# Kernel optimization log

Hardware: AMD Instinct MI355X
Metric: run time of the kernel (lower is better)

The kernel has to match this reference:

```python
import jax, jax.numpy as jnp
import numpy as np

B, T, C, H, W = 1, 16, 320, 16, 16
HEADS, DIM_HEAD, NREG = 8, 40, 1
L = T * H * W  # 4096


def setup_inputs() -> dict:
    key = jax.random.key(0)
    ks = jax.random.split(key, 8)
    features = jax.random.normal(ks[0], (B, T, C, H, W), jnp.float32)
    # epipolar geometry mask: True = attend. randint 0/1 per spec.
    attn_mask = jax.random.randint(ks[1], (B, L, L), 0, 2) == 1
    s = 0.02
    Wq = jax.random.normal(ks[2], (C, HEADS * DIM_HEAD), jnp.float32) * s
    Wk = jax.random.normal(ks[3], (C, HEADS * DIM_HEAD), jnp.float32) * s
    Wv = jax.random.normal(ks[4], (C, HEADS * DIM_HEAD), jnp.float32) * s
    reg_tokens = jax.random.normal(ks[5], (1, NREG, C), jnp.float32)
    Wo = jax.random.normal(ks[6], (HEADS * DIM_HEAD, C), jnp.float32) * s
    bo = jnp.zeros((C,), jnp.float32)
    return {"features": features, "attn_mask": attn_mask, "Wq": Wq, "Wk": Wk,
            "Wv": Wv, "reg_tokens": reg_tokens, "Wo": Wo, "bo": bo}


def reference(features, attn_mask, Wq, Wk, Wv, reg_tokens, Wo, bo):
    b, t, c, h, w = features.shape
    # B T C H W -> B (T H W) C
    x = features.transpose(0, 1, 3, 4, 2).reshape(b, t * h * w, c)
    context = jnp.concatenate(
        [jnp.broadcast_to(reg_tokens, (b, NREG, c)), x], axis=1)
    # pad mask: register tokens always visible (True)
    mask = jnp.pad(attn_mask, ((0, 0), (0, 0), (NREG, 0)), constant_values=True)
    # projections, split heads: B L (H D) -> B H L D
    def heads(y):
        return y.reshape(b, y.shape[1], HEADS, DIM_HEAD).transpose(0, 2, 1, 3)
    q = heads(x @ Wq)
    k = heads(context @ Wk)
    v = heads(context @ Wv)
    scale = DIM_HEAD ** -0.5  # SDPA default scale
    scores = jnp.einsum('bhqd,bhkd->bhqk', q, k) * scale
    neg = jnp.finfo(scores.dtype).min
    scores = jnp.where(mask[:, None, :, :], scores, neg)
    attn = jax.nn.softmax(scores, axis=-1)
    out = jnp.einsum('bhqk,bhkd->bhqd', attn, v)
    out = out.transpose(0, 2, 1, 3).reshape(b, t * h * w, HEADS * DIM_HEAD)
    out = out @ Wo + bo
    # B (T H W) C -> (B H W) T C
    out = out.reshape(b, t, h, w, c).transpose(0, 2, 3, 1, 4)
    return out.reshape(b * h * w, t, c)
```

## Files before the change

kernel.cpp:

```cpp
#include <hip/hip_runtime.h>
#include <hip/hip_bf16.h>
#include <math.h>

#define CDIM 320
#define LQ   4096
#define LKTX 4097
#define NH   8
#define DH   40
#define NWORDS 65
#define NSPLIT 2

typedef __attribute__((ext_vector_type(8))) short short8;
typedef __attribute__((ext_vector_type(4))) float f32x4;

#define QSCALE ((float)(0.15811388300841897 * 1.4426950408889634))


__global__ __launch_bounds__(256) void prep(
    const float* __restrict__ feat, const float* __restrict__ reg,
    const float* __restrict__ Wq, const float* __restrict__ Wk,
    const float* __restrict__ Wv, const float* __restrict__ Wo,
    __hip_bfloat16* __restrict__ ctxb, __hip_bfloat16* __restrict__ Wt,
    __hip_bfloat16* __restrict__ Wot, short* __restrict__ Kpack,
    short* __restrict__ Vpack) {
    __shared__ float xs[64 * 65];
    int b = blockIdx.x, t = threadIdx.x;
    if (b < 320) {
        int tt = b & 15, cg = (b >> 4) % 5, hg = (b >> 4) / 5;
        int c0 = cg * 64, hw0 = hg * 64;
        int cl = t >> 6, hwl = t & 63;
#pragma unroll
        for (int i = 0; i < 16; i++) {
            int c = cl * 16 + i;
            xs[c * 65 + hwl] = feat[(size_t)(tt * CDIM + c0 + c) * 256 + hw0 + hwl];
        }
        __syncthreads();
        int cq = t >> 6;
        int row = tt * 256 + hw0 + hwl;
        short8 v0, v1;
#pragma unroll
        for (int j = 0; j < 8; j++) {
            __hip_bfloat16 b0 = __float2bfloat16(xs[(cq * 16 + j) * 65 + hwl]);
            __hip_bfloat16 b1 = __float2bfloat16(xs[(cq * 16 + 8 + j) * 65 + hwl]);
            v0[j] = *(short*)&b0;
            v1[j] = *(short*)&b1;
        }
        short* dst = (short*)ctxb + (size_t)(1 + row) * CDIM + c0 + cq * 16;
        *(short8*)dst = v0;
        *(short8*)(dst + 8) = v1;
    } else if (b < 1520) {
        int idx = (b - 320) * 256 + t;
        if (idx < 960 * 320) {
            int n = idx / 320, k = idx % 320;
            float v;
            if (n < 320)      v = Wq[k * 320 + n] * QSCALE;
            else if (n < 640) v = Wk[k * 320 + (n - 320)];
            else              v = Wv[k * 320 + (n - 640)];
            Wt[n * 320 + k] = __float2bfloat16(v);
        }
        if (idx < 320 * 320) {
            int n = idx / 320, k = idx % 320;
            Wot[n * 320 + k] = __float2bfloat16(Wo[k * 320 + n]);
        }
        if (idx < 320) ctxb[idx] = __float2bfloat16(reg[idx]);
    } else if (b < 1910) {
        int i = (b - 1520) * 256 + t;
        int R = i / 3, part = i % 3;
        *(uint4*)(Kpack + (size_t)R * 64 + 40 + part * 8) = make_uint4(0, 0, 0, 0);
    } else {
        int i = (b - 1910) * 256 + t;
        int g2 = i >> 6, off = i & 63, r = off >> 3, c8 = off & 7;
        unsigned short hv = (r == 0) ? 0x3F80 : 0;
        unsigned u = hv | ((unsigned)hv << 16);
        *(uint4*)(Vpack + (size_t)g2 * 3072 + (40 + r) * 64 + c8 * 8) =
            make_uint4(u, u, u, u);
    }
}

__global__ __launch_bounds__(256) void mask_pack(const int* __restrict__ mask,
                                                 unsigned long long* __restrict__ packed) {
    int wid = blockIdx.x * 4 + (threadIdx.x >> 6);
    int j = threadIdx.x & 63;
    int q = wid >> 4, g = wid & 15;
    const uint4* m4 = (const uint4*)(mask + (size_t)q * 4096 + g * 256);
    uint4 mv = m4[j];
    unsigned long long b0 = __ballot(mv.x != 0);
    unsigned long long b1 = __ballot(mv.y != 0);
    unsigned long long b2 = __ballot(mv.z != 0);
    unsigned long long b3 = __ballot(mv.w != 0);
    unsigned long long carry =
        (g == 0) ? 1ull : (unsigned long long)(mask[(size_t)q * 4096 + g * 256 - 1] != 0);
    unsigned long long b3s = (b3 << 1) | carry;
    if (j < 4) {
        int sh = j * 16;
        unsigned long long w = ((b3s >> sh) & 0xFFFFull) |
                               (((b0 >> sh) & 0xFFFFull) << 16) |
                               (((b1 >> sh) & 0xFFFFull) << 32) |
                               (((b2 >> sh) & 0xFFFFull) << 48);
        packed[(size_t)q * NWORDS + g * 4 + j] = w;
    }
    if (j == 4 && g == 15) packed[(size_t)q * NWORDS + 64] = b3 >> 63;
}

__global__ __launch_bounds__(256) void qkv_gemm(
    const __hip_bfloat16* __restrict__ Ab, const __hip_bfloat16* __restrict__ Btb,
    __hip_bfloat16* __restrict__ Qb, short* __restrict__ Kpack,
    short* __restrict__ Vpack) {
    __shared__ short As[64 * 72];
    __shared__ short Bs[128 * 72];
    const short* A  = (const short*)Ab;
    const short* Bt = (const short*)Btb;
    int t = threadIdx.x;
    int wv = t >> 6, lane = t & 63, quad = lane >> 4, l16 = lane & 15;
    int m0 = blockIdx.y * 64, n0 = blockIdx.x * 128;

    f32x4 acc[8];
#pragma unroll
    for (int ct = 0; ct < 8; ct++)
#pragma unroll
        for (int r = 0; r < 4; r++) acc[ct][r] = 0.f;

    for (int k0 = 0; k0 < 320; k0 += 64) {
        uint4 av[2], bv[4];
#pragma unroll
        for (int i = 0; i < 2; i++) {
            int c = t + i * 256;
            int row = c >> 3, kc = (c & 7) * 8;
            av[i] = make_uint4(0, 0, 0, 0);
            if (m0 + row < LKTX)
                av[i] = *(const uint4*)(A + (size_t)(m0 + row) * 320 + k0 + kc);
        }
#pragma unroll
        for (int i = 0; i < 4; i++) {
            int c = t + i * 256;
            int row = c >> 3, kc = (c & 7) * 8;
            bv[i] = make_uint4(0, 0, 0, 0);
            if (n0 + row < 960)
                bv[i] = *(const uint4*)(Bt + (size_t)(n0 + row) * 320 + k0 + kc);
        }
        __syncthreads();
#pragma unroll
        for (int i = 0; i < 2; i++) {
            int c = t + i * 256;
            *(uint4*)&As[(c >> 3) * 72 + (c & 7) * 8] = av[i];
        }
#pragma unroll
        for (int i = 0; i < 4; i++) {
            int c = t + i * 256;
            *(uint4*)&Bs[(c >> 3) * 72 + (c & 7) * 8] = bv[i];
        }
        __syncthreads();
        short8 a0 = *(const short8*)&As[(wv * 16 + l16) * 72 + quad * 8];
        short8 a1 = *(const short8*)&As[(wv * 16 + l16) * 72 + 32 + quad * 8];
#pragma unroll
        for (int ct = 0; ct < 8; ct++) {
            short8 b0 = *(const short8*)&Bs[(ct * 16 + l16) * 72 + quad * 8];
            short8 b1 = *(const short8*)&Bs[(ct * 16 + l16) * 72 + 32 + quad * 8];
            acc[ct] = __builtin_amdgcn_mfma_f32_16x16x32_bf16(a0, b0, acc[ct], 0, 0, 0);
            acc[ct] = __builtin_amdgcn_mfma_f32_16x16x32_bf16(a1, b1, acc[ct], 0, 0, 0);
        }
    }

    int by = blockIdx.y;
    int rowK = (quad * 4) * 4 + wv;
    int colV = wv * 4 + quad;
#pragma unroll
    for (int ct = 0; ct < 8; ct++) {
        int n = n0 + ct * 16 + l16;
        if (n >= 960) continue;
        if (n < 320) {
#pragma unroll
            for (int r = 0; r < 4; r++) {
                int m = m0 + wv * 16 + quad * 4 + r;
                if (m >= 1 && m <= LQ) {
                    __hip_bfloat16 o = __float2bfloat16(acc[ct][r]);
                    Qb[(size_t)(m - 1) * 320 + n] = o;
                }
            }
        } else if (n < 640) {
            int nn = n - 320, h = nn / 40, d = nn % 40;
            short* base = Kpack + (((size_t)(h * 65 + by) * 64) * 64 + d);
#pragma unroll
            for (int r = 0; r < 4; r++) {
                __hip_bfloat16 o = __float2bfloat16(acc[ct][r]);
                base[(size_t)(rowK + r * 4) * 64] = *(short*)&o;
            }
        } else {
            int nn = n - 640, h = nn / 40, d = nn % 40;
            short* base = Vpack + (((size_t)(h * 65 + by) * 48 + d) * 64 + colV);
#pragma unroll
            for (int r = 0; r < 4; r++) {
                __hip_bfloat16 o = __float2bfloat16(acc[ct][r]);
                base[r * 16] = *(short*)&o;
            }
        }
    }
}

__global__ __launch_bounds__(256) void flash_attn_mfma(
    const __hip_bfloat16* __restrict__ Qbh, const short* __restrict__ Kpack,
    const short* __restrict__ Vpack, const unsigned long long* __restrict__ packed,
    float* __restrict__ Opart, float* __restrict__ l_arr) {
    __shared__ short Ks[64 * 72];
    __shared__ short Vs[48 * 72];
    __shared__ short Ps[4 * 16 * 72];

    int t = threadIdx.x;
    int wv = t >> 6, lane = t & 63;
    int quad = lane >> 4, l16 = lane & 15;
    int h = blockIdx.y, s = blockIdx.z;
    int l0 = blockIdx.x * 64;
    int q0w = l0 + wv * 16;
    int kt0 = s * 33;
    int nkt = s ? 32 : 33;

    const short* Kt = Kpack + ((size_t)(h * 65 + kt0) << 12);
    const short* Vt = Vpack + (size_t)(h * 65 + kt0) * 3072;
    const unsigned long long* pM = packed + (size_t)(q0w + l16) * NWORDS + kt0;

    short* dK0 = &Ks[(t >> 3) * 72 + (t & 7) * 8];
    short* dK1 = &Ks[(32 + (t >> 3)) * 72 + (t & 7) * 8];
    short* dV0 = &Vs[(t >> 3) * 72 + (t & 7) * 8];
    short* dV1 = &Vs[(32 + (t >> 3)) * 72 + (t & 7) * 8];

    short8 qa0, qa1 = {0, 0, 0, 0, 0, 0, 0, 0};
    {
        const short* qp = (const short*)Qbh + (size_t)(q0w + l16) * 320 + h * DH;
        qa0 = *(const short8*)(qp + quad * 8);
        if (quad == 0) qa1 = *(const short8*)(qp + 32);
    }

    f32x4 accO[3];
#pragma unroll
    for (int dt = 0; dt < 3; dt++)
#pragma unroll
        for (int r = 0; r < 4; r++) accO[dt][r] = 0.f;

    for (int it = 0; it < nkt; it++) {
        uint4 k0 = *(const uint4*)(Kt + t * 8);
        uint4 k1 = *(const uint4*)(Kt + 2048 + t * 8);
        uint4 v0 = *(const uint4*)(Vt + t * 8);
        uint4 v1;
        if (t < 128) v1 = *(const uint4*)(Vt + 2048 + t * 8);
        unsigned long long word = *pM;
        Kt += 4096;
        Vt += 3072;
        pM++;

        __syncthreads();
        *(uint4*)dK0 = k0;
        *(uint4*)dK1 = k1;
        *(uint4*)dV0 = v0;
        if (t < 128) *(uint4*)dV1 = v1;
        __syncthreads();

        f32x4 S[4];
#pragma unroll
        for (int ct = 0; ct < 4; ct++) {
            f32x4 a = {0.f, 0.f, 0.f, 0.f};
            short8 b0 = *(const short8*)&Ks[(ct * 16 + l16) * 72 + quad * 8];
            short8 b1 = *(const short8*)&Ks[(ct * 16 + l16) * 72 + 32 + quad * 8];
            a = __builtin_amdgcn_mfma_f32_16x16x32_bf16(qa0, b0, a, 0, 0, 0);
            a = __builtin_amdgcn_mfma_f32_16x16x32_bf16(qa1, b1, a, 0, 0, 0);
            S[ct] = a;
        }

        int psbase = wv * 16 * 72;
#pragma unroll
        for (int r = 0; r < 4; r++) {
            int rowlane = quad * 4 + r;
            unsigned long long wrd = __shfl(word, rowlane);
            unsigned nib = (unsigned)(wrd >> (l16 * 4)) & 0xFu;
            float p0 = __builtin_amdgcn_exp2f(S[0][r]);
            float p1 = __builtin_amdgcn_exp2f(S[1][r]);
            float p2 = __builtin_amdgcn_exp2f(S[2][r]);
            float p3 = __builtin_amdgcn_exp2f(S[3][r]);
            p0 = (nib & 1u) ? p0 : 0.f;
            p1 = (nib & 2u) ? p1 : 0.f;
            p2 = (nib & 4u) ? p2 : 0.f;
            p3 = (nib & 8u) ? p3 : 0.f;
            unsigned u0 = __float_as_uint(p0) + 0x8000u;
            unsigned u1 = __float_as_uint(p1) + 0x8000u;
            unsigned u2 = __float_as_uint(p2) + 0x8000u;
            unsigned u3 = __float_as_uint(p3) + 0x8000u;
            unsigned lo = (u0 >> 16) | (u1 & 0xFFFF0000u);
            unsigned hi = (u2 >> 16) | (u3 & 0xFFFF0000u);
            *(uint2*)&Ps[psbase + rowlane * 72 + l16 * 4] = make_uint2(lo, hi);
        }

#pragma unroll
        for (int c = 0; c < 2; c++) {
            short8 pa = *(const short8*)&Ps[psbase + l16 * 72 + c * 32 + quad * 8];
#pragma unroll
            for (int dt = 0; dt < 3; dt++) {
                short8 vbf = *(const short8*)&Vs[(dt * 16 + l16) * 72 + c * 32 + quad * 8];
                accO[dt] = __builtin_amdgcn_mfma_f32_16x16x32_bf16(pa, vbf, accO[dt], 0, 0, 0);
            }
        }
    }

#pragma unroll
    for (int r = 0; r < 4; r++) {
        float l_r = __shfl(accO[2][r], quad * 16 + 8);
        int qrow = q0w + quad * 4 + r;
        size_t base = ((size_t)(s * NH + h) * LQ + qrow) * DH;
        Opart[base + l16] = accO[0][r];
        Opart[base + 16 + l16] = accO[1][r];
        if (l16 < 8) Opart[base + 32 + l16] = accO[2][r];
        if (l16 == 0) l_arr[(size_t)(s * NH + h) * LQ + qrow] = l_r;
    }
}

__global__ __launch_bounds__(256) void combine(
    const float* __restrict__ Opart, const float* __restrict__ l_arr,
    __hip_bfloat16* __restrict__ aob) {
    int idx = blockIdx.x * 256 + threadIdx.x;
    if (idx >= NH * LQ * 5) return;
    int dg = idx % 5;
    int hq = idx / 5;
    int q = hq & (LQ - 1), h = hq >> 12;
    size_t r0 = (size_t)h * LQ + q;
    size_t r1 = (size_t)(NH + h) * LQ + q;
    float inv = 1.f / (l_arr[r0] + l_arr[r1]);
    const float* a = &Opart[r0 * DH + dg * 8];
    const float* b = &Opart[r1 * DH + dg * 8];
    short8 o;
#pragma unroll
    for (int j = 0; j < 8; j++) {
        __hip_bfloat16 ob = __float2bfloat16((a[j] + b[j]) * inv);
        o[j] = *(short*)&ob;
    }
    *(short8*)((short*)aob + (size_t)q * CDIM + h * DH + dg * 8) = o;
}

__global__ __launch_bounds__(256) void out_gemm(
    const __hip_bfloat16* __restrict__ Ab, const __hip_bfloat16* __restrict__ Btb,
    float* __restrict__ C, const float* __restrict__ bias) {
    __shared__ short As[64 * 72];
    __shared__ short Bs[64 * 72];
    const short* A  = (const short*)Ab;
    const short* Bt = (const short*)Btb;
    int t = threadIdx.x;
    int wv = t >> 6, lane = t & 63, quad = lane >> 4, l16 = lane & 15;
    int m0 = blockIdx.y * 64, n0 = blockIdx.x * 64;

    f32x4 acc[4];
#pragma unroll
    for (int ct = 0; ct < 4; ct++)
#pragma unroll
        for (int r = 0; r < 4; r++) acc[ct][r] = 0.f;

    for (int k0 = 0; k0 < 320; k0 += 64) {
        uint4 av[2], bv[2];
#pragma unroll
        for (int i = 0; i < 2; i++) {
            int c = t + i * 256;
            int row = c >> 3, kc = (c & 7) * 8;
            av[i] = *(const uint4*)(A + (size_t)(m0 + row) * 320 + k0 + kc);
            bv[i] = *(const uint4*)(Bt + (size_t)(n0 + row) * 320 + k0 + kc);
        }
        __syncthreads();
#pragma unroll
        for (int i = 0; i < 2; i++) {
            int c = t + i * 256;
            *(uint4*)&As[(c >> 3) * 72 + (c & 7) * 8] = av[i];
            *(uint4*)&Bs[(c >> 3) * 72 + (c & 7) * 8] = bv[i];
        }
        __syncthreads();
        short8 a0 = *(const short8*)&As[(wv * 16 + l16) * 72 + quad * 8];
        short8 a1 = *(const short8*)&As[(wv * 16 + l16) * 72 + 32 + quad * 8];
#pragma unroll
        for (int ct = 0; ct < 4; ct++) {
            short8 b0 = *(const short8*)&Bs[(ct * 16 + l16) * 72 + quad * 8];
            short8 b1 = *(const short8*)&Bs[(ct * 16 + l16) * 72 + 32 + quad * 8];
            acc[ct] = __builtin_amdgcn_mfma_f32_16x16x32_bf16(a0, b0, acc[ct], 0, 0, 0);
            acc[ct] = __builtin_amdgcn_mfma_f32_16x16x32_bf16(a1, b1, acc[ct], 0, 0, 0);
        }
    }
#pragma unroll
    for (int ct = 0; ct < 4; ct++)
#pragma unroll
        for (int r = 0; r < 4; r++) {
            int m = m0 + wv * 16 + quad * 4 + r;
            int n = n0 + ct * 16 + l16;
            int rp = (m & 255) * 16 + (m >> 8);
            C[(size_t)rp * CDIM + n] = acc[ct][r] + bias[n];
        }
}

extern "C" void kernel_launch(void* const* d_in, const int* in_sizes, int n_in,
                              void* d_out, int out_size, void* d_ws, size_t ws_size,
                              hipStream_t stream) {
    const float* feat = (const float*)d_in[0];
    const int*   mask = (const int*)d_in[1];
    const float* Wq   = (const float*)d_in[2];
    const float* Wk   = (const float*)d_in[3];
    const float* Wv   = (const float*)d_in[4];
    const float* reg  = (const float*)d_in[5];
    const float* Wo   = (const float*)d_in[6];
    const float* bo   = (const float*)d_in[7];
    float* out = (float*)d_out;

    char* p = (char*)d_ws;
    auto alloc = [&](size_t bytes) {
        char* r = p;
        p += (bytes + 255) & ~(size_t)255;
        return r;
    };
    __hip_bfloat16* ctxb = (__hip_bfloat16*)alloc((size_t)LKTX * CDIM * 2);
    __hip_bfloat16* Wt   = (__hip_bfloat16*)alloc((size_t)960 * 320 * 2);
    __hip_bfloat16* Wot  = (__hip_bfloat16*)alloc((size_t)320 * 320 * 2);
    __hip_bfloat16* Qb   = (__hip_bfloat16*)alloc((size_t)LQ * CDIM * 2);
    short* Kpack = (short*)alloc((size_t)NH * 65 * 64 * 64 * 2);
    short* Vpack = (short*)alloc((size_t)NH * 65 * 48 * 64 * 2);
    unsigned long long* packed = (unsigned long long*)alloc((size_t)LQ * NWORDS * 8);
    float* Opart = (float*)alloc((size_t)NSPLIT * NH * LQ * DH * 4);
    float* l_arr = (float*)alloc((size_t)NSPLIT * NH * LQ * 4);
    __hip_bfloat16* aob  = (__hip_bfloat16*)alloc((size_t)LQ * CDIM * 2);

    prep<<<2040, 256, 0, stream>>>(feat, reg, Wq, Wk, Wv, Wo, ctxb, Wt, Wot,
                                   Kpack, Vpack);
    mask_pack<<<16384, 256, 0, stream>>>(mask, packed);
    qkv_gemm<<<dim3(8, 65), 256, 0, stream>>>(ctxb, Wt, Qb, Kpack, Vpack);
    flash_attn_mfma<<<dim3(64, NH, NSPLIT), 256, 0, stream>>>(Qb, Kpack, Vpack,
                                                              packed, Opart, l_arr);
    combine<<<(NH * LQ * 5 + 255) / 256, 256, 0, stream>>>(Opart, l_arr, aob);
    out_gemm<<<dim3(5, 64), 256, 0, stream>>>(aob, Wot, out, bo);
}
```

Before: 222.0 us.

## Restructure attention pipeline: fuse mask pack into prep, combine into out GEMM, retile flash kernel

Merges the mask-packing kernel into prep and the split-combine step into the output GEMM, dropping two launches and the intermediate bf16 attention buffer. The QKV GEMM now writes a plain row-major 960-wide buffer instead of head-packed K/V tiles, and the flash kernel transposes V into double-buffered shared memory itself. Each wave now handles 32 queries and keeps P in registers, computing S transposed so that P feeds the 16x16x16 MFMA directly with no shared-memory round trip. The key range is split four ways instead of two. Costs include uncoalesced strided K/V loads, scalar transposed V stores to LDS, and more partial-sum traffic in the output GEMM.

```diff
diff --git a/kernel.cpp b/kernel.cpp
--- a/kernel.cpp
+++ b/kernel.cpp
@@ -8,25 +8,53 @@
 #define NH   8
 #define DH   40
 #define NWORDS 65
-#define NSPLIT 2
+#define NSPLIT 4
+#define CBROWS 4224
 
 typedef __attribute__((ext_vector_type(8))) short short8;
+typedef __attribute__((ext_vector_type(4))) short short4v;
 typedef __attribute__((ext_vector_type(4))) float f32x4;
 
+#define MFMA16(a, b, c) __builtin_amdgcn_mfma_f32_16x16x16bf16_1k(a, b, c, 0, 0, 0)
+#define MFMA32(a, b, c) __builtin_amdgcn_mfma_f32_16x16x32_bf16(a, b, c, 0, 0, 0)
+
 #define QSCALE ((float)(0.15811388300841897 * 1.4426950408889634))
-
 
 __global__ __launch_bounds__(256) void prep(
     const float* __restrict__ feat, const float* __restrict__ reg,
     const float* __restrict__ Wq, const float* __restrict__ Wk,
     const float* __restrict__ Wv, const float* __restrict__ Wo,
+    const int* __restrict__ mask, unsigned long long* __restrict__ packed,
     __hip_bfloat16* __restrict__ ctxb, __hip_bfloat16* __restrict__ Wt,
-    __hip_bfloat16* __restrict__ Wot, short* __restrict__ Kpack,
-    short* __restrict__ Vpack) {
+    __hip_bfloat16* __restrict__ Wot) {
     __shared__ float xs[64 * 65];
     int b = blockIdx.x, t = threadIdx.x;
-    if (b < 320) {
-        int tt = b & 15, cg = (b >> 4) % 5, hg = (b >> 4) / 5;
+    if (b < 16384) {
+        int wid = b * 4 + (t >> 6);
+        int j = t & 63;
+        int q = wid >> 4, g = wid & 15;
+        const uint4* m4 = (const uint4*)(mask + (size_t)q * 4096 + g * 256);
+        uint4 mv = m4[j];
+        unsigned long long b0 = __ballot(mv.x != 0);
+        unsigned long long b1 = __ballot(mv.y != 0);
+        unsigned long long b2 = __ballot(mv.z != 0);
+        unsigned long long b3 = __ballot(mv.w != 0);
+        unsigned long long carry =
+            (g == 0) ? 1ull
+                     : (unsigned long long)(mask[(size_t)q * 4096 + g * 256 - 1] != 0);
+        unsigned long long b3s = (b3 << 1) | carry;
+        if (j < 4) {
+            int sh = j * 16;
+            unsigned long long w = ((b3s >> sh) & 0xFFFFull) |
+                                   (((b0 >> sh) & 0xFFFFull) << 16) |
+                                   (((b1 >> sh) & 0xFFFFull) << 32) |
+                                   (((b2 >> sh) & 0xFFFFull) << 48);
+            packed[(size_t)q * NWORDS + g * 4 + j] = w;
+        }
+        if (j == 4 && g == 15) packed[(size_t)q * NWORDS + 64] = b3 >> 63;
+    } else if (b < 16704) {
+        int bb = b - 16384;
+        int tt = bb & 15, cg = (bb >> 4) % 5, hg = (bb >> 4) / 5;
         int c0 = cg * 64, hw0 = hg * 64;
         int cl = t >> 6, hwl = t & 63;
 #pragma unroll
@@ -48,8 +76,8 @@
         short* dst = (short*)ctxb + (size_t)(1 + row) * CDIM + c0 + cq * 16;
         *(short8*)dst = v0;
         *(short8*)(dst + 8) = v1;
-    } else if (b < 1520) {
-        int idx = (b - 320) * 256 + t;
+    } else {
+        int idx = (b - 16704) * 256 + t;
         if (idx < 960 * 320) {
             int n = idx / 320, k = idx % 320;
             float v;
@@ -63,49 +91,12 @@
             Wot[n * 320 + k] = __float2bfloat16(Wo[k * 320 + n]);
         }
         if (idx < 320) ctxb[idx] = __float2bfloat16(reg[idx]);
-    } else if (b < 1910) {
-        int i = (b - 1520) * 256 + t;
-        int R = i / 3, part = i % 3;
-        *(uint4*)(Kpack + (size_t)R * 64 + 40 + part * 8) = make_uint4(0, 0, 0, 0);
-    } else {
-        int i = (b - 1910) * 256 + t;
-        int g2 = i >> 6, off = i & 63, r = off >> 3, c8 = off & 7;
-        unsigned short hv = (r == 0) ? 0x3F80 : 0;
-        unsigned u = hv | ((unsigned)hv << 16);
-        *(uint4*)(Vpack + (size_t)g2 * 3072 + (40 + r) * 64 + c8 * 8) =
-            make_uint4(u, u, u, u);
-    }
-}
-
-__global__ __launch_bounds__(256) void mask_pack(const int* __restrict__ mask,
-                                                 unsigned long long* __restrict__ packed) {
-    int wid = blockIdx.x * 4 + (threadIdx.x >> 6);
-    int j = threadIdx.x & 63;
-    int q = wid >> 4, g = wid & 15;
-    const uint4* m4 = (const uint4*)(mask + (size_t)q * 4096 + g * 256);
-    uint4 mv = m4[j];
-    unsigned long long b0 = __ballot(mv.x != 0);
-    unsigned long long b1 = __ballot(mv.y != 0);
-    unsigned long long b2 = __ballot(mv.z != 0);
-    unsigned long long b3 = __ballot(mv.w != 0);
-    unsigned long long carry =
-        (g == 0) ? 1ull : (unsigned long long)(mask[(size_t)q * 4096 + g * 256 - 1] != 0);
-    unsigned long long b3s = (b3 << 1) | carry;
-    if (j < 4) {
-        int sh = j * 16;
-        unsigned long long w = ((b3s >> sh) & 0xFFFFull) |
-                               (((b0 >> sh) & 0xFFFFull) << 16) |
-                               (((b1 >> sh) & 0xFFFFull) << 32) |
-                               (((b2 >> sh) & 0xFFFFull) << 48);
-        packed[(size_t)q * NWORDS + g * 4 + j] = w;
-    }
-    if (j == 4 && g == 15) packed[(size_t)q * NWORDS + 64] = b3 >> 63;
+    }
 }
 
 __global__ __launch_bounds__(256) void qkv_gemm(
     const __hip_bfloat16* __restrict__ Ab, const __hip_bfloat16* __restrict__ Btb,
-    __hip_bfloat16* __restrict__ Qb, short* __restrict__ Kpack,
-    short* __restrict__ Vpack) {
+    __hip_bfloat16* __restrict__ Cbo) {
     __shared__ short As[64 * 72];
     __shared__ short Bs[128 * 72];
     const short* A  = (const short*)Ab;
@@ -156,190 +147,179 @@
         for (int ct = 0; ct < 8; ct++) {
             short8 b0 = *(const short8*)&Bs[(ct * 16 + l16) * 72 + quad * 8];
             short8 b1 = *(const short8*)&Bs[(ct * 16 + l16) * 72 + 32 + quad * 8];
-            acc[ct] = __builtin_amdgcn_mfma_f32_16x16x32_bf16(a0, b0, acc[ct], 0, 0, 0);
-            acc[ct] = __builtin_amdgcn_mfma_f32_16x16x32_bf16(a1, b1, acc[ct], 0, 0, 0);
-        }
-    }
-
-    int by = blockIdx.y;
-    int rowK = (quad * 4) * 4 + wv;
-    int colV = wv * 4 + quad;
-#pragma unroll
-    for (int ct = 0; ct < 8; ct++) {
-        int n = n0 + ct * 16 + l16;
-        if (n >= 960) continue;
-        if (n < 320) {
-#pragma unroll
-            for (int r = 0; r < 4; r++) {
-                int m = m0 + wv * 16 + quad * 4 + r;
-                if (m >= 1 && m <= LQ) {
-                    __hip_bfloat16 o = __float2bfloat16(acc[ct][r]);
-                    Qb[(size_t)(m - 1) * 320 + n] = o;
-                }
-            }
-        } else if (n < 640) {
-            int nn = n - 320, h = nn / 40, d = nn % 40;
-            short* base = Kpack + (((size_t)(h * 65 + by) * 64) * 64 + d);
-#pragma unroll
-            for (int r = 0; r < 4; r++) {
-                __hip_bfloat16 o = __float2bfloat16(acc[ct][r]);
-                base[(size_t)(rowK + r * 4) * 64] = *(short*)&o;
-            }
-        } else {
-            int nn = n - 640, h = nn / 40, d = nn % 40;
-            short* base = Vpack + (((size_t)(h * 65 + by) * 48 + d) * 64 + colV);
-#pragma unroll
-            for (int r = 0; r < 4; r++) {
-                __hip_bfloat16 o = __float2bfloat16(acc[ct][r]);
-                base[r * 16] = *(short*)&o;
-            }
-        }
-    }
+            acc[ct] = MFMA32(a0, b0, acc[ct]);
+            acc[ct] = MFMA32(a1, b1, acc[ct]);
+        }
+        __syncthreads();
+    }
+#pragma unroll
+    for (int ct = 0; ct < 8; ct++)
+#pragma unroll
+        for (int r = 0; r < 4; r++) {
+            int m = m0 + wv * 16 + quad * 4 + r;
+            int n = n0 + ct * 16 + l16;
+            if (n < 960)
+                Cbo[(size_t)m * 960 + n] = __float2bfloat16(acc[ct][r]);
+        }
 }
 
-__global__ __launch_bounds__(256) void flash_attn_mfma(
-    const __hip_bfloat16* __restrict__ Qbh, const short* __restrict__ Kpack,
-    const short* __restrict__ Vpack, const unsigned long long* __restrict__ packed,
+__global__ __launch_bounds__(256, 4) void flash_attn(
+    const __hip_bfloat16* __restrict__ Cbh,
+    const unsigned long long* __restrict__ packed,
     float* __restrict__ Opart, float* __restrict__ l_arr) {
-    __shared__ short Ks[64 * 72];
-    __shared__ short Vs[48 * 72];
-    __shared__ short Ps[4 * 16 * 72];
+    __shared__ short Ks[2 * 64 * 72];
+    __shared__ short Vs[2 * 48 * 72];
 
     int t = threadIdx.x;
     int wv = t >> 6, lane = t & 63;
     int quad = lane >> 4, l16 = lane & 15;
     int h = blockIdx.y, s = blockIdx.z;
-    int l0 = blockIdx.x * 64;
-    int q0w = l0 + wv * 16;
-    int kt0 = s * 33;
-    int nkt = s ? 32 : 33;
-
-    const short* Kt = Kpack + ((size_t)(h * 65 + kt0) << 12);
-    const short* Vt = Vpack + (size_t)(h * 65 + kt0) * 3072;
-    const unsigned long long* pM = packed + (size_t)(q0w + l16) * NWORDS + kt0;
-
-    short* dK0 = &Ks[(t >> 3) * 72 + (t & 7) * 8];
-    short* dK1 = &Ks[(32 + (t >> 3)) * 72 + (t & 7) * 8];
-    short* dV0 = &Vs[(t >> 3) * 72 + (t & 7) * 8];
-    short* dV1 = &Vs[(32 + (t >> 3)) * 72 + (t & 7) * 8];
-
-    short8 qa0, qa1 = {0, 0, 0, 0, 0, 0, 0, 0};
-    {
-        const short* qp = (const short*)Qbh + (size_t)(q0w + l16) * 320 + h * DH;
-        qa0 = *(const short8*)(qp + quad * 8);
-        if (quad == 0) qa1 = *(const short8*)(qp + 32);
-    }
-
-    f32x4 accO[3];
-#pragma unroll
-    for (int dt = 0; dt < 3; dt++)
-#pragma unroll
-        for (int r = 0; r < 4; r++) accO[dt][r] = 0.f;
+    int q0 = blockIdx.x * 128 + wv * 32;
+    int kt0 = (s == 0) ? 0 : 16 * s + 1;
+    int nkt = s ? 16 : 17;
+    const short* Cb = (const short*)Cbh;
+
+    for (int i = t; i < 64 * 24; i += 256) {
+        int rr = i / 24, c = 40 + i % 24;
+        Ks[rr * 72 + c] = 0;
+        Ks[4608 + rr * 72 + c] = 0;
+    }
+    for (int i = t; i < 8 * 72; i += 256) {
+        int rr = i / 72, c = i % 72;
+        short v = (rr == 0 && c < 64) ? (short)0x3F80 : (short)0;
+        Vs[(40 + rr) * 72 + c] = v;
+        Vs[3456 + (40 + rr) * 72 + c] = v;
+    }
+
+    short8 qa[2][2];
+#pragma unroll
+    for (int qs = 0; qs < 2; qs++) {
+        const short* qp = Cb + (size_t)(q0 + qs * 16 + l16 + 1) * 960 + h * DH;
+        qa[qs][0] = *(const short8*)(qp + quad * 8);
+        short8 z = {0, 0, 0, 0, 0, 0, 0, 0};
+        qa[qs][1] = (quad == 0) ? *(const short8*)(qp + 32) : z;
+    }
+
+    int key0 = t / 5, cc0 = t - 5 * key0;
+    int t2 = t + 256;
+    int key1 = t2 / 5, cc1 = t2 - 5 * key1;
+    bool has2 = (t < 64);
+    const short* pK0 = Cb + (size_t)(kt0 * 64 + key0) * 960 + 320 + h * DH + cc0 * 8;
+    const short* pV0 = Cb + (size_t)(kt0 * 64 + key0) * 960 + 640 + h * DH + cc0 * 8;
+    const short* pK1 = Cb + (size_t)(kt0 * 64 + key1) * 960 + 320 + h * DH + cc1 * 8;
+    const short* pV1 = Cb + (size_t)(kt0 * 64 + key1) * 960 + 640 + h * DH + cc1 * 8;
+    const unsigned long long* pM0 = packed + (size_t)(q0 + l16) * NWORDS + kt0;
+    const unsigned long long* pM1 = packed + (size_t)(q0 + 16 + l16) * NWORDS + kt0;
+
+    uint4 rk0 = *(const uint4*)pK0;  pK0 += 61440;
+    uint4 rv0 = *(const uint4*)pV0;  pV0 += 61440;
+    uint4 rk1 = make_uint4(0, 0, 0, 0), rv1 = make_uint4(0, 0, 0, 0);
+    if (has2) { rk1 = *(const uint4*)pK1; rv1 = *(const uint4*)pV1; }
+    pK1 += 61440; pV1 += 61440;
+    unsigned long long wq0 = *pM0++;
+    unsigned long long wq1 = *pM1++;
+
+    f32x4 accO[2][3];
+#pragma unroll
+    for (int qs = 0; qs < 2; qs++)
+#pragma unroll
+        for (int dt = 0; dt < 3; dt++)
+#pragma unroll
+            for (int r = 0; r < 4; r++) accO[qs][dt][r] = 0.f;
 
     for (int it = 0; it < nkt; it++) {
-        uint4 k0 = *(const uint4*)(Kt + t * 8);
-        uint4 k1 = *(const uint4*)(Kt + 2048 + t * 8);
-        uint4 v0 = *(const uint4*)(Vt + t * 8);
-        uint4 v1;
-        if (t < 128) v1 = *(const uint4*)(Vt + 2048 + t * 8);
-        unsigned long long word = *pM;
-        Kt += 4096;
-        Vt += 3072;
-        pM++;
-
-        __syncthreads();
-        *(uint4*)dK0 = k0;
-        *(uint4*)dK1 = k1;
-        *(uint4*)dV0 = v0;
-        if (t < 128) *(uint4*)dV1 = v1;
-        __syncthreads();
-
-        f32x4 S[4];
+        int ko = (it & 1) * 4608, vo = (it & 1) * 3456;
+        *(uint4*)&Ks[ko + key0 * 72 + cc0 * 8] = rk0;
+        {
+            const short* ds = (const short*)&rv0;
+#pragma unroll
+            for (int u = 0; u < 8; u++) Vs[vo + (cc0 * 8 + u) * 72 + key0] = ds[u];
+        }
+        if (has2) {
+            *(uint4*)&Ks[ko + key1 * 72 + cc1 * 8] = rk1;
+            const short* ds = (const short*)&rv1;
+#pragma unroll
+            for (int u = 0; u < 8; u++) Vs[vo + (cc1 * 8 + u) * 72 + key1] = ds[u];
+        }
+        unsigned long long mw0 = wq0, mw1 = wq1;
+        rk0 = *(const uint4*)pK0;  pK0 += 61440;
+        rv0 = *(const uint4*)pV0;  pV0 += 61440;
+        if (has2) { rk1 = *(const uint4*)pK1; rv1 = *(const uint4*)pV1; }
+        pK1 += 61440; pV1 += 61440;
+        wq0 = *pM0++;
+        wq1 = *pM1++;
+        __syncthreads();
+
+        const short* KB = &Ks[ko];
+        const short* VB = &Vs[vo];
+        unsigned lo[2], hi[2];
+        lo[0] = (unsigned)(mw0 >> quad);
+        hi[0] = (unsigned)(mw0 >> (quad + 32));
+        lo[1] = (unsigned)(mw1 >> quad);
+        hi[1] = (unsigned)(mw1 >> (quad + 32));
+
+        short4v pf[2][4];
 #pragma unroll
         for (int ct = 0; ct < 4; ct++) {
-            f32x4 a = {0.f, 0.f, 0.f, 0.f};
-            short8 b0 = *(const short8*)&Ks[(ct * 16 + l16) * 72 + quad * 8];
-            short8 b1 = *(const short8*)&Ks[(ct * 16 + l16) * 72 + 32 + quad * 8];
-            a = __builtin_amdgcn_mfma_f32_16x16x32_bf16(qa0, b0, a, 0, 0, 0);
-            a = __builtin_amdgcn_mfma_f32_16x16x32_bf16(qa1, b1, a, 0, 0, 0);
-            S[ct] = a;
-        }
-
-        int psbase = wv * 16 * 72;
-#pragma unroll
-        for (int r = 0; r < 4; r++) {
-            int rowlane = quad * 4 + r;
-            unsigned long long wrd = __shfl(word, rowlane);
-            unsigned nib = (unsigned)(wrd >> (l16 * 4)) & 0xFu;
-            float p0 = __builtin_amdgcn_exp2f(S[0][r]);
-            float p1 = __builtin_amdgcn_exp2f(S[1][r]);
-            float p2 = __builtin_amdgcn_exp2f(S[2][r]);
-            float p3 = __builtin_amdgcn_exp2f(S[3][r]);
-            p0 = (nib & 1u) ? p0 : 0.f;
-            p1 = (nib & 2u) ? p1 : 0.f;
-            p2 = (nib & 4u) ? p2 : 0.f;
-            p3 = (nib & 8u) ? p3 : 0.f;
-            unsigned u0 = __float_as_uint(p0) + 0x8000u;
-            unsigned u1 = __float_as_uint(p1) + 0x8000u;
-            unsigned u2 = __float_as_uint(p2) + 0x8000u;
-            unsigned u3 = __float_as_uint(p3) + 0x8000u;
-            unsigned lo = (u0 >> 16) | (u1 & 0xFFFF0000u);
-            unsigned hi = (u2 >> 16) | (u3 & 0xFFFF0000u);
-            *(uint2*)&Ps[psbase + rowlane * 72 + l16 * 4] = make_uint2(lo, hi);
-        }
-
-#pragma unroll
-        for (int c = 0; c < 2; c++) {
-            short8 pa = *(const short8*)&Ps[psbase + l16 * 72 + c * 32 + quad * 8];
-#pragma unroll
-            for (int dt = 0; dt < 3; dt++) {
-                short8 vbf = *(const short8*)&Vs[(dt * 16 + l16) * 72 + c * 32 + quad * 8];
-                accO[dt] = __builtin_amdgcn_mfma_f32_16x16x32_bf16(pa, vbf, accO[dt], 0, 0, 0);
+            short8 kb0 = *(const short8*)&KB[(ct * 16 + l16) * 72 + quad * 8];
+            short8 kb1 = *(const short8*)&KB[(ct * 16 + l16) * 72 + 32 + quad * 8];
+#pragma unroll
+            for (int qs = 0; qs < 2; qs++) {
+                f32x4 S = {0.f, 0.f, 0.f, 0.f};
+                S = MFMA32(kb0, qa[qs][0], S);
+                S = MFMA32(kb1, qa[qs][1], S);
+                float p0 = __builtin_amdgcn_exp2f(S[0]);
+                float p1 = __builtin_amdgcn_exp2f(S[1]);
+                float p2 = __builtin_amdgcn_exp2f(S[2]);
+                float p3 = __builtin_amdgcn_exp2f(S[3]);
+                p0 = ((lo[qs] >> (4 * ct)) & 1u) ? p0 : 0.f;
+                p1 = ((lo[qs] >> (4 * ct + 16)) & 1u) ? p1 : 0.f;
+                p2 = ((hi[qs] >> (4 * ct)) & 1u) ? p2 : 0.f;
+                p3 = ((hi[qs] >> (4 * ct + 16)) & 1u) ? p3 : 0.f;
+                unsigned u0 = __float_as_uint(p0) + 0x8000u;
+                unsigned u1 = __float_as_uint(p1) + 0x8000u;
+                unsigned u2 = __float_as_uint(p2) + 0x8000u;
+                unsigned u3 = __float_as_uint(p3) + 0x8000u;
+                uint2 pk = make_uint2((u0 >> 16) | (u1 & 0xFFFF0000u),
+                                      (u2 >> 16) | (u3 & 0xFFFF0000u));
+                pf[qs][ct] = *(short4v*)&pk;
             }
         }
-    }
-
-#pragma unroll
-    for (int r = 0; r < 4; r++) {
-        float l_r = __shfl(accO[2][r], quad * 16 + 8);
-        int qrow = q0w + quad * 4 + r;
-        size_t base = ((size_t)(s * NH + h) * LQ + qrow) * DH;
-        Opart[base + l16] = accO[0][r];
-        Opart[base + 16 + l16] = accO[1][r];
-        if (l16 < 8) Opart[base + 32 + l16] = accO[2][r];
-        if (l16 == 0) l_arr[(size_t)(s * NH + h) * LQ + qrow] = l_r;
+
+#pragma unroll
+        for (int dt = 0; dt < 3; dt++) {
+#pragma unroll
+            for (int ct = 0; ct < 4; ct++) {
+                short4v vf = *(const short4v*)&VB[(dt * 16 + l16) * 72 + ct * 16 + quad * 4];
+                accO[0][dt] = MFMA16(vf, pf[0][ct], accO[0][dt]);
+                accO[1][dt] = MFMA16(vf, pf[1][ct], accO[1][dt]);
+            }
+        }
+    }
+
+#pragma unroll
+    for (int qs = 0; qs < 2; qs++) {
+        int q = q0 + qs * 16 + l16;
+        size_t base = ((size_t)(s * NH + h) * LQ + q) * DH;
+        float4 f0 = make_float4(accO[qs][0][0], accO[qs][0][1], accO[qs][0][2], accO[qs][0][3]);
+        float4 f1 = make_float4(accO[qs][1][0], accO[qs][1][1], accO[qs][1][2], accO[qs][1][3]);
+        *(float4*)&Opart[base + quad * 4] = f0;
+        *(float4*)&Opart[base + 16 + quad * 4] = f1;
+        if (quad < 2) {
+            float4 f2 = make_float4(accO[qs][2][0], accO[qs][2][1], accO[qs][2][2], accO[qs][2][3]);
+            *(float4*)&Opart[base + 32 + quad * 4] = f2;
+        }
+        if (quad == 2) l_arr[(size_t)(s * NH + h) * LQ + q] = accO[qs][2][0];
     }
 }
 
-__global__ __launch_bounds__(256) void combine(
+__global__ __launch_bounds__(256) void out_gemm(
     const float* __restrict__ Opart, const float* __restrict__ l_arr,
-    __hip_bfloat16* __restrict__ aob) {
-    int idx = blockIdx.x * 256 + threadIdx.x;
-    if (idx >= NH * LQ * 5) return;
-    int dg = idx % 5;
-    int hq = idx / 5;
-    int q = hq & (LQ - 1), h = hq >> 12;
-    size_t r0 = (size_t)h * LQ + q;
-    size_t r1 = (size_t)(NH + h) * LQ + q;
-    float inv = 1.f / (l_arr[r0] + l_arr[r1]);
-    const float* a = &Opart[r0 * DH + dg * 8];
-    const float* b = &Opart[r1 * DH + dg * 8];
-    short8 o;
-#pragma unroll
-    for (int j = 0; j < 8; j++) {
-        __hip_bfloat16 ob = __float2bfloat16((a[j] + b[j]) * inv);
-        o[j] = *(short*)&ob;
-    }
-    *(short8*)((short*)aob + (size_t)q * CDIM + h * DH + dg * 8) = o;
-}
-
-__global__ __launch_bounds__(256) void out_gemm(
-    const __hip_bfloat16* __restrict__ Ab, const __hip_bfloat16* __restrict__ Btb,
-    float* __restrict__ C, const float* __restrict__ bias) {
+    const __hip_bfloat16* __restrict__ Wotb, float* __restrict__ C,
+    const float* __restrict__ bias) {
     __shared__ short As[64 * 72];
     __shared__ short Bs[64 * 72];
-    const short* A  = (const short*)Ab;
-    const short* Bt = (const short*)Btb;
+    const short* Bt = (const short*)Wotb;
     int t = threadIdx.x;
     int wv = t >> 6, lane = t & 63, quad = lane >> 4, l16 = lane & 15;
     int m0 = blockIdx.y * 64, n0 = blockIdx.x * 64;
@@ -350,21 +330,43 @@
 #pragma unroll
         for (int r = 0; r < 4; r++) acc[ct][r] = 0.f;
 
-    for (int k0 = 0; k0 < 320; k0 += 64) {
+    for (int k0 = 0; k0 < 5; k0++) {
         uint4 av[2], bv[2];
 #pragma unroll
         for (int i = 0; i < 2; i++) {
-            int c = t + i * 256;
-            int row = c >> 3, kc = (c & 7) * 8;
-            av[i] = *(const uint4*)(A + (size_t)(m0 + row) * 320 + k0 + kc);
-            bv[i] = *(const uint4*)(Bt + (size_t)(n0 + row) * 320 + k0 + kc);
+            int cidx = t + i * 256;
+            int row = cidx >> 3, cl = (cidx & 7) * 8;
+            int c = k0 * 64 + cl;
+            int hh = c / 40, d = c % 40;
+            int q = m0 + row;
+            float ls = 0.f;
+            float vals[8] = {0, 0, 0, 0, 0, 0, 0, 0};
+#pragma unroll
+            for (int sp = 0; sp < NSPLIT; sp++) {
+                size_t rbase = ((size_t)(sp * NH + hh) * LQ + q) * DH + d;
+                float4 a = *(const float4*)&Opart[rbase];
+                float4 b = *(const float4*)&Opart[rbase + 4];
+                vals[0] += a.x; vals[1] += a.y; vals[2] += a.z; vals[3] += a.w;
+                vals[4] += b.x; vals[5] += b.y; vals[6] += b.z; vals[7] += b.w;
+                ls += l_arr[(size_t)(sp * NH + hh) * LQ + q];
+            }
+            float inv = 1.f / ls;
+            unsigned pk[4];
+#pragma unroll
+            for (int u = 0; u < 4; u++) {
+                unsigned e0 = __float_as_uint(vals[2 * u] * inv) + 0x8000u;
+                unsigned e1 = __float_as_uint(vals[2 * u + 1] * inv) + 0x8000u;
+                pk[u] = (e0 >> 16) | (e1 & 0xFFFF0000u);
+            }
+            av[i] = make_uint4(pk[0], pk[1], pk[2], pk[3]);
+            bv[i] = *(const uint4*)(Bt + (size_t)(n0 + row) * 320 + k0 * 64 + cl);
         }
         __syncthreads();
 #pragma unroll
         for (int i = 0; i < 2; i++) {
-            int c = t + i * 256;
-            *(uint4*)&As[(c >> 3) * 72 + (c & 7) * 8] = av[i];
-            *(uint4*)&Bs[(c >> 3) * 72 + (c & 7) * 8] = bv[i];
+            int cidx = t + i * 256;
+            *(uint4*)&As[(cidx >> 3) * 72 + (cidx & 7) * 8] = av[i];
+            *(uint4*)&Bs[(cidx >> 3) * 72 + (cidx & 7) * 8] = bv[i];
         }
         __syncthreads();
         short8 a0 = *(const short8*)&As[(wv * 16 + l16) * 72 + quad * 8];
@@ -373,9 +375,10 @@
         for (int ct = 0; ct < 4; ct++) {
             short8 b0 = *(const short8*)&Bs[(ct * 16 + l16) * 72 + quad * 8];
             short8 b1 = *(const short8*)&Bs[(ct * 16 + l16) * 72 + 32 + quad * 8];
-            acc[ct] = __builtin_amdgcn_mfma_f32_16x16x32_bf16(a0, b0, acc[ct], 0, 0, 0);
-            acc[ct] = __builtin_amdgcn_mfma_f32_16x16x32_bf16(a1, b1, acc[ct], 0, 0, 0);
-        }
+            acc[ct] = MFMA32(a0, b0, acc[ct]);
+            acc[ct] = MFMA32(a1, b1, acc[ct]);
+        }
+        __syncthreads();
     }
 #pragma unroll
     for (int ct = 0; ct < 4; ct++)
@@ -408,22 +411,17 @@
         return r;
     };
     __hip_bfloat16* ctxb = (__hip_bfloat16*)alloc((size_t)LKTX * CDIM * 2);
+    __hip_bfloat16* Cb   = (__hip_bfloat16*)alloc((size_t)CBROWS * 960 * 2);
     __hip_bfloat16* Wt   = (__hip_bfloat16*)alloc((size_t)960 * 320 * 2);
     __hip_bfloat16* Wot  = (__hip_bfloat16*)alloc((size_t)320 * 320 * 2);
-    __hip_bfloat16* Qb   = (__hip_bfloat16*)alloc((size_t)LQ * CDIM * 2);
-    short* Kpack = (short*)alloc((size_t)NH * 65 * 64 * 64 * 2);
-    short* Vpack = (short*)alloc((size_t)NH * 65 * 48 * 64 * 2);
-    unsigned long long* packed = (unsigned long long*)alloc((size_t)LQ * NWORDS * 8);
+    unsigned long long* packed =
+        (unsigned long long*)alloc(((size_t)LQ * NWORDS + 64) * 8);
     float* Opart = (float*)alloc((size_t)NSPLIT * NH * LQ * DH * 4);
     float* l_arr = (float*)alloc((size_t)NSPLIT * NH * LQ * 4);
-    __hip_bfloat16* aob  = (__hip_bfloat16*)alloc((size_t)LQ * CDIM * 2);
-
-    prep<<<2040, 256, 0, stream>>>(feat, reg, Wq, Wk, Wv, Wo, ctxb, Wt, Wot,
-                                   Kpack, Vpack);
-    mask_pack<<<16384, 256, 0, stream>>>(mask, packed);
-    qkv_gemm<<<dim3(8, 65), 256, 0, stream>>>(ctxb, Wt, Qb, Kpack, Vpack);
-    flash_attn_mfma<<<dim3(64, NH, NSPLIT), 256, 0, stream>>>(Qb, Kpack, Vpack,
-                                                              packed, Opart, l_arr);
-    combine<<<(NH * LQ * 5 + 255) / 256, 256, 0, stream>>>(Opart, l_arr, aob);
-    out_gemm<<<dim3(5, 64), 256, 0, stream>>>(aob, Wot, out, bo);
+
+    prep<<<17904, 256, 0, stream>>>(feat, reg, Wq, Wk, Wv, Wo, mask, packed,
+                                    ctxb, Wt, Wot);
+    qkv_gemm<<<dim3(8, 65), 256, 0, stream>>>(ctxb, Wt, Cb);
+    flash_attn<<<dim3(32, NH, NSPLIT), 256, 0, stream>>>(Cb, packed, Opart, l_arr);
+    out_gemm<<<dim3(5, 64), 256, 0, stream>>>(Opart, l_arr, Wot, out, bo);
 }
```

New measurement: 221.3 us. About the same (-0.3%).
